# Kernel tuning notes

Measured on AMD Instinct MI355X. Metric: run time of the kernel, lower is better.

The kernel has to match this reference:

```python
import jax, jax.numpy as jnp
import numpy as np

VOCAB, EMBED, HIDDEN, PAD = 32000, 512, 1024, 3

def setup_inputs() -> dict:
    key = jax.random.key(0)
    ks = jax.random.split(key, 7)
    B, S = 16, 256
    input_ids = jax.random.randint(ks[0], (B, S), 0, VOCAB)
    hidden = jnp.zeros((B, HIDDEN), dtype=jnp.float32)
    sc = 0.02
    emb_table = jax.random.normal(ks[1], (VOCAB, EMBED), jnp.float32) * sc
    Wxh_w = jax.random.normal(ks[2], (HIDDEN, EMBED), jnp.float32) * sc
    Wxh_b = jax.random.normal(ks[3], (HIDDEN,), jnp.float32) * sc
    Whh_w = jax.random.normal(ks[4], (HIDDEN, HIDDEN), jnp.float32) * sc
    Who_w = jax.random.normal(ks[5], (VOCAB, HIDDEN), jnp.float32) * sc
    Who_b = jax.random.normal(ks[6], (VOCAB,), jnp.float32) * sc
    return {"input_ids": input_ids, "hidden": hidden, "emb_table": emb_table,
            "Wxh_w": Wxh_w, "Wxh_b": Wxh_b, "Whh_w": Whh_w,
            "Who_w": Who_w, "Who_b": Who_b}

def reference(input_ids, hidden, emb_table, Wxh_w, Wxh_b, Whh_w, Who_w, Who_b):
    # padding_idx: row PAD of the embedding is zero
    pad_mask = (jnp.arange(VOCAB) != PAD).astype(emb_table.dtype)
    table = emb_table * pad_mask[:, None]
    embeds = table[input_ids]                      # [B, S, E]
    # precompute input projection for all steps: [B, S, H]
    xproj = jnp.einsum('bse,he->bsh', embeds, Wxh_w) + Wxh_b

    def step(h, xp_t):                             # xp_t: [B, H]
        h_new = jnp.tanh(xp_t + h @ Whh_w.T)
        return h_new, h_new

    h_final, h_all = jax.lax.scan(step, hidden, jnp.swapaxes(xproj, 0, 1))
    # h_all: [S, B, H] -> logits [B, S, V]
    logits = jnp.einsum('sbh,vh->bsv', h_all, Who_w) + Who_b
    return (logits, h_final)
```

## Files before the change

### kernel.cpp

```cpp
#include <hip/hip_runtime.h>
#include <stdint.h>

#define NB 16
#define NS 256
#define NV 32000
#define NE 512
#define NH 1024
#define PAD_IDX 3

#define WS_XP    0L
#define WS_HCH   16777216L
#define WS_WHO   25198592L
#define WS_FLG   90734592L
#define WS_NEED  90800384L

typedef __attribute__((ext_vector_type(8))) short bf16x8;
typedef __attribute__((ext_vector_type(4))) float f32x4;
typedef __attribute__((ext_vector_type(4))) uint32_t u32x4;

__device__ __forceinline__ uint16_t f2bf(float f){
  union { float f; uint32_t u; } v; v.f = f;
  return (uint16_t)((v.u + 0x7fffu + ((v.u >> 16) & 1u)) >> 16);
}

__device__ __forceinline__ bf16x8 pack8(float4 a, float4 b){
  bf16x8 r;
  r[0]=(short)f2bf(a.x); r[1]=(short)f2bf(a.y); r[2]=(short)f2bf(a.z); r[3]=(short)f2bf(a.w);
  r[4]=(short)f2bf(b.x); r[5]=(short)f2bf(b.y); r[6]=(short)f2bf(b.z); r[7]=(short)f2bf(b.w);
  return r;
}

__device__ __forceinline__ u32x4 load_coh16(const void* p){
  u32x4 r;
  asm volatile("global_load_dwordx4 %0, %1, off sc0 sc1" : "=v"(r) : "v"(p) : "memory");
  return r;
}
__device__ __forceinline__ uint32_t load_coh4(const void* p){
  uint32_t r;
  asm volatile("global_load_dword %0, %1, off sc0 sc1" : "=v"(r) : "v"(p) : "memory");
  return r;
}
__device__ __forceinline__ void store_coh8(void* p, uint64_t v){
  asm volatile("global_store_dwordx2 %0, %1, off sc0 sc1" :: "v"(p), "v"(v) : "memory");
}
__device__ __forceinline__ void store_coh4(void* p, uint32_t v){
  asm volatile("global_store_dword %0, %1, off sc0 sc1" :: "v"(p), "v"(v) : "memory");
}
__device__ __forceinline__ void store_nt4(void* p, float v){
  asm volatile("global_store_dword %0, %1, off nt" :: "v"(p), "v"(v) : "memory");
}

__device__ __forceinline__ u32x4 umax4(u32x4 a, u32x4 b){
  u32x4 r;
  r[0] = a[0] > b[0] ? a[0] : b[0];
  r[1] = a[1] > b[1] ? a[1] : b[1];
  r[2] = a[2] > b[2] ? a[2] : b[2];
  r[3] = a[3] > b[3] ? a[3] : b[3];
  return r;
}

__device__ __forceinline__ float tanh_fast(float x){
  x = fminf(fmaxf(x, -10.f), 10.f);
  float t = __builtin_amdgcn_exp2f(x * 2.885390081777927f);
  return (t - 1.0f) * __builtin_amdgcn_rcpf(t + 1.0f);
}

__global__ void k_init(const float* __restrict__ hidden, uint16_t* __restrict__ hch,
                       uint32_t* __restrict__ flg){
  long idx = (long)blockIdx.x * 256 + threadIdx.x;
  ((u32x4*)(hch + (long)NB * NH))[idx] = (u32x4){~0u, ~0u, ~0u, ~0u};
  if (idx < NB * NH) hch[idx] = f2bf(hidden[idx]);
  if (idx < 512) flg[idx] = 0u;
}

__global__ void k_cvt(const float* __restrict__ src, uint32_t* __restrict__ dst){
  long idx = (long)blockIdx.x * 256 + threadIdx.x;
  const float4* p = (const float4*)src;
  float4 a = p[idx*2], b = p[idx*2+1];
  u32x4 d;
  d[0] = (uint32_t)f2bf(a.x) | ((uint32_t)f2bf(a.y) << 16);
  d[1] = (uint32_t)f2bf(a.z) | ((uint32_t)f2bf(a.w) << 16);
  d[2] = (uint32_t)f2bf(b.x) | ((uint32_t)f2bf(b.y) << 16);
  d[3] = (uint32_t)f2bf(b.z) | ((uint32_t)f2bf(b.w) << 16);
  ((u32x4*)dst)[idx] = d;
}

__global__ __launch_bounds__(256) void k_xproj(
    const int* __restrict__ ids, const float* __restrict__ tab,
    const float* __restrict__ wxh, const float* __restrict__ bxh,
    float* __restrict__ xp){
  int bid = blockIdx.x;
  int tm = bid & 63, tn = bid >> 6;
  int Mb = tm * 64, Nb = tn * 64;
  int tid = threadIdx.x;
  int w = tid >> 6, l = tid & 63;
  int lr = l & 15, lk = l >> 4;

  int m = Mb + w*16 + lr;
  int id = ids[m];
  const float* arow = tab + (long)id * NE;
  bool pad = (id == PAD_IDX);

  f32x4 acc[4];
  #pragma unroll
  for (int j = 0; j < 4; ++j) acc[j] = (f32x4){0.f,0.f,0.f,0.f};

  for (int k0 = 0; k0 < NE; k0 += 32){
    int k = k0 + lk*8;
    bf16x8 af = (bf16x8){0,0,0,0,0,0,0,0};
    if (!pad){
      float4 a = *(const float4*)(arow + k);
      float4 b = *(const float4*)(arow + k + 4);
      af = pack8(a, b);
    }
    #pragma unroll
    for (int j = 0; j < 4; ++j){
      const float* brow = wxh + (long)(Nb + j*16 + lr) * NE + k;
      float4 x = *(const float4*)brow;
      float4 y = *(const float4*)(brow + 4);
      bf16x8 bf_ = pack8(x, y);
      acc[j] = __builtin_amdgcn_mfma_f32_16x16x32_bf16(af, bf_, acc[j], 0, 0, 0);
    }
  }
  #pragma unroll
  for (int j = 0; j < 4; ++j){
    int n = Nb + j*16 + lr;
    float bias = bxh[n];
    #pragma unroll
    for (int r = 0; r < 4; ++r){
      int row = Mb + w*16 + lk*4 + r;
      xp[(long)row * NH + n] = acc[j][r] + bias;
    }
  }
}

__global__ __launch_bounds__(256, 2) void k_fused(
    const float* __restrict__ whh, const float* __restrict__ xp,
    uint16_t* __restrict__ hch, const uint16_t* __restrict__ whobf,
    const float* __restrict__ whob, uint32_t* __restrict__ allvis,
    uint32_t* __restrict__ fin, float* __restrict__ out,
    float* __restrict__ hfin){
  __shared__ __align__(16) char smem[35*1024];
  const int bid = blockIdx.x;
  const int tid = threadIdx.x;

  if (bid < 16){
    uint16_t* hlds = (uint16_t*)smem;
    uint16_t* hs2  = (uint16_t*)(smem + 32768);
    const int wv = tid >> 6, l = tid & 63;
    const int lr = l & 15, lk = l >> 4;
    const int base = bid*64 + wv*16;
    __builtin_amdgcn_s_setprio(2);

    bf16x8 wf[32];
    #pragma unroll
    for (int kk = 0; kk < 32; ++kk){
      const float* s0 = whh + (long)(base + lr) * NH + kk*32 + lk*8;
      wf[kk] = pack8(*(const float4*)s0, *(const float4*)(s0 + 4));
    }

    float xpreg[4];
    #pragma unroll
    for (int r = 0; r < 4; ++r)
      xpreg[r] = xp[((long)(lk*4 + r) * NS + 0) * NH + base + lr];

    for (int t = 0; t < NS; ++t){
      {
        const char* ps = (const char*)hch + ((long)t * NB + (l >> 2)) * 2048
                       + wv*512 + (l & 3)*128;
        u32x4 hf[8];
        while (true){
          #pragma unroll
          for (int j = 0; j < 8; ++j) hf[j] = load_coh16(ps + j*16);
          asm volatile("s_waitcnt vmcnt(0)" ::: "memory");
          __builtin_amdgcn_sched_barrier(0);
          u32x4 m4 = hf[0];
          #pragma unroll
          for (int j = 1; j < 8; ++j) m4 = umax4(m4, hf[j]);
          uint32_t m01 = m4[0] > m4[1] ? m4[0] : m4[1];
          uint32_t m23 = m4[2] > m4[3] ? m4[2] : m4[3];
          uint32_t m = m01 > m23 ? m01 : m23;
          if (__all(m != 0xFFFFFFFFu)) break;
        }
        __builtin_amdgcn_sched_barrier(0);
        int batch = l >> 2;
        #pragma unroll
        for (int j = 0; j < 8; ++j){
          int cib = wv*32 + (l & 3)*8 + j;
          ((u32x4*)hlds)[batch*128 + (cib ^ (batch & 7))] = hf[j];
        }
      }
      __syncthreads();
      if (bid == 0 && tid == 0) store_coh4(allvis + t, 1u);

      f32x4 a0 = (f32x4){0.f,0.f,0.f,0.f}, a1 = a0;
      #pragma unroll
      for (int kk = 0; kk < 32; kk += 2){
        bf16x8 af0 = *(const bf16x8*)&((const u32x4*)hlds)[lr*128 + (( kk   *4 + lk) ^ (lr & 7))];
        bf16x8 af1 = *(const bf16x8*)&((const u32x4*)hlds)[lr*128 + (((kk+1)*4 + lk) ^ (lr & 7))];
        a0 = __builtin_amdgcn_mfma_f32_16x16x32_bf16(af0, wf[kk  ], a0, 0, 0, 0);
        a1 = __builtin_amdgcn_mfma_f32_16x16x32_bf16(af1, wf[kk+1], a1, 0, 0, 0);
      }
      f32x4 acc = a0 + a1;

      #pragma unroll
      for (int r = 0; r < 4; ++r){
        float hv = tanh_fast(xpreg[r] + acc[r]);
        hs2[(lk*4 + r)*64 + wv*16 + lr] = f2bf(hv);
        if (t == NS-1) hfin[(long)(lk*4 + r) * NH + base + lr] = hv;
      }
      __syncthreads();

      {
        int row = tid >> 4, ch = tid & 15;
        uint64_t v = *(const uint64_t*)&hs2[row*64 + ch*4];
        char* dst = (char*)hch + ((long)(t+1) * NB + row) * 2048 + (bid*64 + ch*4)*2;
        store_coh8(dst, v);
      }
      if (t + 1 < NS){
        #pragma unroll
        for (int r = 0; r < 4; ++r)
          xpreg[r] = xp[((long)(lk*4 + r) * NS + (t+1)) * NH + base + lr];
      }
    }
    asm volatile("s_waitcnt vmcnt(0)" ::: "memory");
    __syncthreads();
    if (tid == 0) store_coh4(fin + bid, 1u);
    return;
  }

  uint16_t* As = (uint16_t*)smem;
  uint16_t* Bs = (uint16_t*)(smem + 8192);
  int tile = bid - 16;
  int tm = tile / 250;
  int tn = tile % 250;
  int Mb = tm * 128, Nb = tn * 128;
  int hs = tm * 8 + 8;

  if (hs < 256){
    while (true){
      uint32_t f = load_coh4(allvis + hs);
      asm volatile("s_waitcnt vmcnt(0)" ::: "memory");
      __builtin_amdgcn_sched_barrier(0);
      if (__syncthreads_count(f == 0u) == 0) break;
      __builtin_amdgcn_s_sleep(16);
    }
  } else {
    const uint32_t* gp = fin + (tid & 15);
    while (true){
      uint32_t f = load_coh4(gp);
      asm volatile("s_waitcnt vmcnt(0)" ::: "memory");
      __builtin_amdgcn_sched_barrier(0);
      if (__syncthreads_count(f == 0u) == 0) break;
      __builtin_amdgcn_s_sleep(16);
    }
  }

  int wv = tid >> 6, l = tid & 63;
  int wm = wv >> 1, wn = wv & 1;
  int lr = l & 15, lk = l >> 4;

  int r0 = tid >> 2, c0 = tid & 3;
  int r1 = r0 + 64;
  const uint16_t* pa0 = hch + (long)(Mb + r0 + 16) * NH + c0*8;
  const uint16_t* pa1 = hch + (long)(Mb + r1 + 16) * NH + c0*8;
  const uint16_t* pb0 = whobf + (long)(Nb + r0) * NH + c0*8;
  const uint16_t* pb1 = whobf + (long)(Nb + r1) * NH + c0*8;
  int da0 = r0*4 + (c0 ^ (r0 & 3));
  int da1 = r1*4 + (c0 ^ (r1 & 3));

  u32x4 ra0 = *(const u32x4*)pa0;
  u32x4 ra1 = *(const u32x4*)pa1;
  u32x4 rb0 = *(const u32x4*)pb0;
  u32x4 rb1 = *(const u32x4*)pb1;

  f32x4 acc[4][4];
  #pragma unroll
  for (int i = 0; i < 4; ++i)
    #pragma unroll
    for (int jj = 0; jj < 4; ++jj) acc[i][jj] = (f32x4){0.f,0.f,0.f,0.f};

  for (int kt = 0; kt < 32; ++kt){
    ((u32x4*)As)[da0] = ra0;
    ((u32x4*)As)[da1] = ra1;
    ((u32x4*)Bs)[da0] = rb0;
    ((u32x4*)Bs)[da1] = rb1;
    __syncthreads();
    if (kt != 31){
      int off = (kt + 1) * 32;
      ra0 = *(const u32x4*)(pa0 + off);
      ra1 = *(const u32x4*)(pa1 + off);
      rb0 = *(const u32x4*)(pb0 + off);
      rb1 = *(const u32x4*)(pb1 + off);
    }
    bf16x8 af[4], bg_[4];
    #pragma unroll
    for (int i = 0; i < 4; ++i){
      int ra = wm*64 + i*16 + lr;
      int rb = wn*64 + i*16 + lr;
      af[i]  = *(const bf16x8*)&((const u32x4*)As)[ra*4 + (lk ^ (ra & 3))];
      bg_[i] = *(const bf16x8*)&((const u32x4*)Bs)[rb*4 + (lk ^ (rb & 3))];
    }
    #pragma unroll
    for (int i = 0; i < 4; ++i)
      #pragma unroll
      for (int jj = 0; jj < 4; ++jj)
        acc[i][jj] = __builtin_amdgcn_mfma_f32_16x16x32_bf16(af[i], bg_[jj], acc[i][jj], 0, 0, 0);
    __syncthreads();
  }

  #pragma unroll
  for (int jj = 0; jj < 4; ++jj){
    int col = Nb + wn*64 + jj*16 + lr;
    float bias = whob[col];
    #pragma unroll
    for (int i = 0; i < 4; ++i){
      #pragma unroll
      for (int rr = 0; rr < 4; ++rr){
        int m = Mb + wm*64 + i*16 + lk*4 + rr;
        long orow = (long)((m & 15) * 256 + (m >> 4));
        store_nt4(&out[orow * NV + col], acc[i][jj][rr] + bias);
      }
    }
  }
}

extern "C" void kernel_launch(void* const* d_in, const int* in_sizes, int n_in,
                              void* d_out, int out_size, void* d_ws, size_t ws_size,
                              hipStream_t stream){
  (void)in_sizes; (void)n_in; (void)out_size;
  if (ws_size < (size_t)WS_NEED) return;

  const int*   ids    = (const int*)  d_in[0];
  const float* hidden = (const float*)d_in[1];
  const float* table  = (const float*)d_in[2];
  const float* wxh    = (const float*)d_in[3];
  const float* bxh    = (const float*)d_in[4];
  const float* whh    = (const float*)d_in[5];
  const float* who    = (const float*)d_in[6];
  const float* whob   = (const float*)d_in[7];

  char* ws = (char*)d_ws;
  float*    xp     = (float*)   (ws + WS_XP);
  uint16_t* hchain = (uint16_t*)(ws + WS_HCH);
  uint16_t* whobf  = (uint16_t*)(ws + WS_WHO);
  uint32_t* allvis = (uint32_t*)(ws + WS_FLG);
  uint32_t* fin    = allvis + 260;
  float* out    = (float*)d_out;
  float* hfinal = out + (long)NB * NS * NV;

  k_init <<<2048,  256, 0, stream>>>(hidden, hchain, allvis);
  k_cvt  <<<16000, 256, 0, stream>>>(who, (uint32_t*)whobf);
  k_xproj<<<1024,  256, 0, stream>>>(ids, table, wxh, bxh, xp);
  k_fused<<<8016,  256, 0, stream>>>(whh, xp, hchain, whobf, whob,
                                     allvis, fin, out, hfinal);
}
```

Measured before the change: 1.002 ms.

## Halve recurrent blocks to 512 threads and pair logits GEMM tiles per block

The serial recurrence now runs on 8 workgroups of 512 threads, each owning 128 hidden units, instead of 16 workgroups of 256 threads. This halves the number of blocks that must publish and poll the shared hidden-state chain each timestep. The aim is to cut cross-block synchronization latency on the critical path, at the cost of more per-step work on each CU. The output-projection GEMM blocks are also widened to 512 threads, so each block computes two 128x128 tiles in separate LDS halves and waits on the larger of their readiness flags. That wait can hold back the earlier tile, and the shared __syncthreads couples the two tiles' progress.

```diff
diff --git a/kernel.cpp b/kernel.cpp
--- a/kernel.cpp
+++ b/kernel.cpp
@@ -134,22 +134,22 @@
   }
 }
 
-__global__ __launch_bounds__(256, 2) void k_fused(
+__global__ __launch_bounds__(512) void k_fused(
     const float* __restrict__ whh, const float* __restrict__ xp,
     uint16_t* __restrict__ hch, const uint16_t* __restrict__ whobf,
     const float* __restrict__ whob, uint32_t* __restrict__ allvis,
     uint32_t* __restrict__ fin, float* __restrict__ out,
     float* __restrict__ hfin){
-  __shared__ __align__(16) char smem[35*1024];
+  __shared__ __align__(16) char smem[37*1024];
   const int bid = blockIdx.x;
   const int tid = threadIdx.x;
 
-  if (bid < 16){
+  if (bid < 8){
     uint16_t* hlds = (uint16_t*)smem;
     uint16_t* hs2  = (uint16_t*)(smem + 32768);
     const int wv = tid >> 6, l = tid & 63;
     const int lr = l & 15, lk = l >> 4;
-    const int base = bid*64 + wv*16;
+    const int base = bid*128 + wv*16;
     __builtin_amdgcn_s_setprio(2);
 
     bf16x8 wf[32];
@@ -164,30 +164,29 @@
     for (int r = 0; r < 4; ++r)
       xpreg[r] = xp[((long)(lk*4 + r) * NS + 0) * NH + base + lr];
 
+    const int pbat = tid >> 5;
+    const int pch  = tid & 31;
+
     for (int t = 0; t < NS; ++t){
       {
-        const char* ps = (const char*)hch + ((long)t * NB + (l >> 2)) * 2048
-                       + wv*512 + (l & 3)*128;
-        u32x4 hf[8];
+        const char* ps = (const char*)hch + ((long)t * NB + pbat) * 2048 + pch*64;
+        u32x4 hf[4];
         while (true){
           #pragma unroll
-          for (int j = 0; j < 8; ++j) hf[j] = load_coh16(ps + j*16);
+          for (int j = 0; j < 4; ++j) hf[j] = load_coh16(ps + j*16);
           asm volatile("s_waitcnt vmcnt(0)" ::: "memory");
           __builtin_amdgcn_sched_barrier(0);
-          u32x4 m4 = hf[0];
-          #pragma unroll
-          for (int j = 1; j < 8; ++j) m4 = umax4(m4, hf[j]);
+          u32x4 m4 = umax4(umax4(hf[0], hf[1]), umax4(hf[2], hf[3]));
           uint32_t m01 = m4[0] > m4[1] ? m4[0] : m4[1];
           uint32_t m23 = m4[2] > m4[3] ? m4[2] : m4[3];
           uint32_t m = m01 > m23 ? m01 : m23;
           if (__all(m != 0xFFFFFFFFu)) break;
         }
         __builtin_amdgcn_sched_barrier(0);
-        int batch = l >> 2;
         #pragma unroll
-        for (int j = 0; j < 8; ++j){
-          int cib = wv*32 + (l & 3)*8 + j;
-          ((u32x4*)hlds)[batch*128 + (cib ^ (batch & 7))] = hf[j];
+        for (int j = 0; j < 4; ++j){
+          int cib = pch*4 + j;
+          ((u32x4*)hlds)[pbat*128 + (cib ^ (pbat & 7))] = hf[j];
         }
       }
       __syncthreads();
@@ -206,15 +205,15 @@
       #pragma unroll
       for (int r = 0; r < 4; ++r){
         float hv = tanh_fast(xpreg[r] + acc[r]);
-        hs2[(lk*4 + r)*64 + wv*16 + lr] = f2bf(hv);
+        hs2[(lk*4 + r)*128 + wv*16 + lr] = f2bf(hv);
         if (t == NS-1) hfin[(long)(lk*4 + r) * NH + base + lr] = hv;
       }
       __syncthreads();
 
       {
-        int row = tid >> 4, ch = tid & 15;
-        uint64_t v = *(const uint64_t*)&hs2[row*64 + ch*4];
-        char* dst = (char*)hch + ((long)(t+1) * NB + row) * 2048 + (bid*64 + ch*4)*2;
+        int row = tid >> 5, ch = tid & 31;
+        uint64_t v = *(const uint64_t*)&hs2[row*128 + ch*4];
+        char* dst = (char*)hch + ((long)(t+1) * NB + row) * 2048 + bid*256 + ch*8;
         store_coh8(dst, v);
       }
       if (t + 1 < NS){
@@ -229,15 +228,19 @@
     return;
   }
 
-  uint16_t* As = (uint16_t*)smem;
-  uint16_t* Bs = (uint16_t*)(smem + 8192);
-  int tile = bid - 16;
+  int sub = tid >> 8;
+  int st  = tid & 255;
+  uint16_t* As = (uint16_t*)(smem + sub*16384);
+  uint16_t* Bs = (uint16_t*)(smem + sub*16384 + 8192);
+  int gbid = bid - 8;
+  int tile = gbid*2 + sub;
   int tm = tile / 250;
   int tn = tile % 250;
   int Mb = tm * 128, Nb = tn * 128;
-  int hs = tm * 8 + 8;
-
-  if (hs < 256){
+  int tmmax = (gbid*2 + 1) / 250;
+
+  if (tmmax < 31){
+    int hs = tmmax * 8 + 8;
     while (true){
       uint32_t f = load_coh4(allvis + hs);
       asm volatile("s_waitcnt vmcnt(0)" ::: "memory");
@@ -246,7 +249,7 @@
       __builtin_amdgcn_s_sleep(16);
     }
   } else {
-    const uint32_t* gp = fin + (tid & 15);
+    const uint32_t* gp = fin + (tid & 7);
     while (true){
       uint32_t f = load_coh4(gp);
       asm volatile("s_waitcnt vmcnt(0)" ::: "memory");
@@ -256,11 +259,11 @@
     }
   }
 
-  int wv = tid >> 6, l = tid & 63;
+  int wv = st >> 6, l = st & 63;
   int wm = wv >> 1, wn = wv & 1;
   int lr = l & 15, lk = l >> 4;
 
-  int r0 = tid >> 2, c0 = tid & 3;
+  int r0 = st >> 2, c0 = st & 3;
   int r1 = r0 + 64;
   const uint16_t* pa0 = hch + (long)(Mb + r0 + 16) * NH + c0*8;
   const uint16_t* pa1 = hch + (long)(Mb + r1 + 16) * NH + c0*8;
@@ -352,6 +355,6 @@
   k_init <<<2048,  256, 0, stream>>>(hidden, hchain, allvis);
   k_cvt  <<<16000, 256, 0, stream>>>(who, (uint32_t*)whobf);
   k_xproj<<<1024,  256, 0, stream>>>(ids, table, wxh, bxh, xp);
-  k_fused<<<8016,  256, 0, stream>>>(whh, xp, hchain, whobf, whob,
+  k_fused<<<4008,  512, 0, stream>>>(whh, xp, hchain, whobf, whob,
                                      allvis, fin, out, hfinal);
 }
```

New measurement: 947.9 us (median of 2 runs). 5.4% less time.
